# Kernel optimization log

Hardware: AMD Instinct MI355X
Metric: run time of the kernel (lower is better)

Reference implementation:

```python
import jax, jax.numpy as jnp
import numpy as np

LAT = (4, 24, 24, 24, 24, 3, 3)  # [mu, L0, L1, L2, L3, 3, 3]


def setup_inputs() -> dict:
    key = jax.random.key(0)
    k1, k2 = jax.random.split(key)
    U_re = jax.random.normal(k1, LAT, dtype=jnp.float32)
    U_im = jax.random.normal(k2, LAT, dtype=jnp.float32)
    return {"U_re": U_re, "U_im": U_im}


def _polyakov_dir(Umu, axis, L):
    """P(x) = prod_{k=0}^{L-1} U_mu(x + k*mu_hat) via a sequential scan of
    batched 3x3 complex matmuls. Umu: [L0,L1,L2,L3,3,3] complex."""

    def step(carry, _):
        P, Ush = carry
        Ush = jnp.roll(Ush, -1, axis=axis)  # U_mu(x + (k)*mu_hat)
        P = jnp.einsum('...ij,...jk->...ik', P, Ush)
        return (P, Ush), None

    (P, _), _ = jax.lax.scan(step, (Umu, Umu), None, length=L - 1)
    return P


def reference(U_re, U_im):
    U = jax.lax.complex(U_re, U_im)  # complex64 link field
    loops = jnp.stack([
        _polyakov_dir(U[mu], mu, U.shape[1 + mu]) for mu in range(4)
    ])  # [4, L0, L1, L2, L3, 3, 3] complex
    # return real/imag stacked so output is a real array
    return jnp.stack([loops.real, loops.imag])
```

## Files before the change

kernel.cpp:

```cpp
#include <hip/hip_runtime.h>

#define LSIZE 24
#define VOL (LSIZE*LSIZE*LSIZE*LSIZE)
#define NLINES (LSIZE*LSIZE*LSIZE)
#define CHUNK 3
#define TPL 8
#define LPB 32
#define TPB 256

__device__ __forceinline__ void cmul(const float* __restrict__ ar, const float* __restrict__ ai,
                                     const float* __restrict__ br, const float* __restrict__ bi,
                                     float* __restrict__ or_, float* __restrict__ oi_) {
#pragma unroll
  for (int i = 0; i < 3; ++i) {
#pragma unroll
    for (int j = 0; j < 3; ++j) {
      float sr = 0.f, si = 0.f;
#pragma unroll
      for (int m = 0; m < 3; ++m) {
        float x = ar[i*3+m], y = ai[i*3+m];
        float u = br[m*3+j], v = bi[m*3+j];
        sr = fmaf(x, u, sr);
        sr = fmaf(-y, v, sr);
        si = fmaf(x, v, si);
        si = fmaf(y, u, si);
      }
      or_[i*3+j] = sr;
      oi_[i*3+j] = si;
    }
  }
}

__device__ __forceinline__ void cp9(float* dr, float* di, const float* sr, const float* si) {
#pragma unroll
  for (int e = 0; e < 9; ++e) { dr[e] = sr[e]; di[e] = si[e]; }
}

__device__ __forceinline__ void setid(float* r, float* im) {
#pragma unroll
  for (int e = 0; e < 9; ++e) { r[e] = (e == 0 || e == 4 || e == 8) ? 1.f : 0.f; im[e] = 0.f; }
}

__device__ __forceinline__ void shup(float* dr, float* di, const float* sr, const float* si, int delta) {
#pragma unroll
  for (int e = 0; e < 9; ++e) {
    dr[e] = __shfl_up(sr[e], (unsigned)delta, 64);
    di[e] = __shfl_up(si[e], (unsigned)delta, 64);
  }
}
__device__ __forceinline__ void shdn(float* dr, float* di, const float* sr, const float* si, int delta) {
#pragma unroll
  for (int e = 0; e < 9; ++e) {
    dr[e] = __shfl_down(sr[e], (unsigned)delta, 64);
    di[e] = __shfl_down(si[e], (unsigned)delta, 64);
  }
}

__global__ __launch_bounds__(TPB, 2) void polyakov_chunk(
    const float* __restrict__ U_re, const float* __restrict__ U_im,
    float* __restrict__ out) {
  const int lane = threadIdx.x & 63;
  const int wv   = threadIdx.x >> 6;
  const int lineBase = blockIdx.x * LPB + wv * (64 / TPL);
  const int mu = lineBase / NLINES;

  int tl, ll, sh;
  if (mu == 3) { tl = lane & 7; ll = lane >> 3; sh = 1; }
  else         { tl = lane >> 3; ll = lane & 7; sh = 8; }

  const int L  = lineBase + ll;
  const int l  = L - mu * NLINES;
  const int cC = l % LSIZE;
  const int cB = (l / LSIZE) % LSIZE;
  const int cA = l / (LSIZE*LSIZE);

  int x0, x1, x2, x3, st;
  if (mu == 0)      { x0 = 0;  x1 = cA; x2 = cB; x3 = cC; st = LSIZE*LSIZE*LSIZE; }
  else if (mu == 1) { x0 = cA; x1 = 0;  x2 = cB; x3 = cC; st = LSIZE*LSIZE; }
  else if (mu == 2) { x0 = cA; x1 = cB; x2 = 0;  x3 = cC; st = LSIZE; }
  else              { x0 = cA; x1 = cB; x2 = cC; x3 = 0;  st = 1; }
  const int s0 = ((x0*LSIZE + x1)*LSIZE + x2)*LSIZE + x3;
  const int k0 = tl * CHUNK;

  const float* __restrict__ bR = U_re + (size_t)mu * (VOL*9);
  const float* __restrict__ bI = U_im + (size_t)mu * (VOL*9);

  float U0r[9], U0i[9], U1r[9], U1i[9], U2r[9], U2i[9];
  {
    const float* p = bR + (size_t)(s0 + (k0+0)*st) * 9;
    const float* q = bI + (size_t)(s0 + (k0+0)*st) * 9;
#pragma unroll
    for (int e = 0; e < 9; ++e) { U0r[e] = p[e]; U0i[e] = q[e]; }
  }
  {
    const float* p = bR + (size_t)(s0 + (k0+1)*st) * 9;
    const float* q = bI + (size_t)(s0 + (k0+1)*st) * 9;
#pragma unroll
    for (int e = 0; e < 9; ++e) { U1r[e] = p[e]; U1i[e] = q[e]; }
  }
  {
    const float* p = bR + (size_t)(s0 + (k0+2)*st) * 9;
    const float* q = bI + (size_t)(s0 + (k0+2)*st) * 9;
#pragma unroll
    for (int e = 0; e < 9; ++e) { U2r[e] = p[e]; U2i[e] = q[e]; }
  }

  float A1r[9], A1i[9], Br[9], Bi[9], S1r[9], S1i[9];
  cmul(U0r, U0i, U1r, U1i, A1r, A1i);
  cmul(A1r, A1i, U2r, U2i, Br,  Bi);
  cmul(U1r, U1i, U2r, U2i, S1r, S1i);

  float Tr[9], Ti[9], Yr[9], Yi[9];

  float Xr[9], Xi[9];
  cp9(Xr, Xi, Br, Bi);
#pragma unroll
  for (int d = 1; d < TPL; d <<= 1) {
    shup(Yr, Yi, Xr, Xi, d * sh);
    if (tl >= d) { cmul(Yr, Yi, Xr, Xi, Tr, Ti); cp9(Xr, Xi, Tr, Ti); }
  }

  float Zr[9], Zi[9];
  cp9(Zr, Zi, Br, Bi);
#pragma unroll
  for (int d = 1; d < TPL; d <<= 1) {
    shdn(Yr, Yi, Zr, Zi, d * sh);
    if (tl + d < TPL) { cmul(Zr, Zi, Yr, Yi, Tr, Ti); cp9(Zr, Zi, Tr, Ti); }
  }

  float Pr[9], Pi[9], Qr[9], Qi[9];
  shup(Pr, Pi, Xr, Xi, sh);
  if (tl == 0) setid(Pr, Pi);
  shdn(Qr, Qi, Zr, Zi, sh);
  if (tl == TPL - 1) setid(Qr, Qi);

  float Rr[9], Ri[9];
  cmul(Qr, Qi, Pr, Pi, Rr, Ri);

  float* oR = out + (size_t)mu * (VOL*9);
  float* oI = out + (size_t)(4 + mu) * (VOL*9);
  float Wr[9], Wi[9];

  cmul(Br, Bi, Rr, Ri, Tr, Ti);
  {
    float* pr = oR + (size_t)(s0 + (k0+0)*st) * 9;
    float* pi = oI + (size_t)(s0 + (k0+0)*st) * 9;
#pragma unroll
    for (int e = 0; e < 9; ++e) { pr[e] = Tr[e]; pi[e] = Ti[e]; }
  }
  cmul(Rr, Ri, U0r, U0i, Tr, Ti);
  cmul(S1r, S1i, Tr, Ti, Wr, Wi);
  {
    float* pr = oR + (size_t)(s0 + (k0+1)*st) * 9;
    float* pi = oI + (size_t)(s0 + (k0+1)*st) * 9;
#pragma unroll
    for (int e = 0; e < 9; ++e) { pr[e] = Wr[e]; pi[e] = Wi[e]; }
  }
  cmul(Rr, Ri, A1r, A1i, Tr, Ti);
  cmul(U2r, U2i, Tr, Ti, Wr, Wi);
  {
    float* pr = oR + (size_t)(s0 + (k0+2)*st) * 9;
    float* pi = oI + (size_t)(s0 + (k0+2)*st) * 9;
#pragma unroll
    for (int e = 0; e < 9; ++e) { pr[e] = Wr[e]; pi[e] = Wi[e]; }
  }
}

extern "C" void kernel_launch(void* const* d_in, const int* in_sizes, int n_in,
                              void* d_out, int out_size, void* d_ws, size_t ws_size,
                              hipStream_t stream) {
  const float* U_re = (const float*)d_in[0];
  const float* U_im = (const float*)d_in[1];
  float* out = (float*)d_out;
  int nblocks = 4 * NLINES / LPB;
  hipLaunchKernelGGL(polyakov_chunk, dim3(nblocks), dim3(TPB), 0, stream, U_re, U_im, out);
}
```

Measured before the change: 197.0 us.

## Stage outputs through LDS for coalesced stores and reload links to cut registers

For mu 0-2, each wave writes its 3x3 results into padded shared memory and then stores them so that adjacent lanes write contiguous 9-float runs, instead of each thread writing strided 36-byte chunks. The link matrices are reloaded from global memory after the scan rather than held in registers across it, and launch bounds rise to 4 blocks per CU to raise occupancy. The cost is extra LDS traffic, waitcnt barriers and repeated global loads, which the cache should mostly serve.

```diff
diff --git a/kernel.cpp b/kernel.cpp
--- a/kernel.cpp
+++ b/kernel.cpp
@@ -3,10 +3,10 @@
 #define LSIZE 24
 #define VOL (LSIZE*LSIZE*LSIZE*LSIZE)
 #define NLINES (LSIZE*LSIZE*LSIZE)
-#define CHUNK 3
-#define TPL 8
 #define LPB 32
 #define TPB 256
+#define ESTRIDE 71
+#define BUFW (18*ESTRIDE)
 
 __device__ __forceinline__ void cmul(const float* __restrict__ ar, const float* __restrict__ ai,
                                      const float* __restrict__ br, const float* __restrict__ bi,
@@ -56,20 +56,21 @@
   }
 }
 
-__global__ __launch_bounds__(TPB, 2) void polyakov_chunk(
+__global__ __launch_bounds__(TPB, 4) void polyakov_hyb(
     const float* __restrict__ U_re, const float* __restrict__ U_im,
     float* __restrict__ out) {
+  __shared__ float buf[4 * BUFW];
+
   const int lane = threadIdx.x & 63;
   const int wv   = threadIdx.x >> 6;
-  const int lineBase = blockIdx.x * LPB + wv * (64 / TPL);
-  const int mu = lineBase / NLINES;
+  const int mu   = (blockIdx.x * LPB) / NLINES;
 
   int tl, ll, sh;
   if (mu == 3) { tl = lane & 7; ll = lane >> 3; sh = 1; }
   else         { tl = lane >> 3; ll = lane & 7; sh = 8; }
 
-  const int L  = lineBase + ll;
-  const int l  = L - mu * NLINES;
+  const int l0 = blockIdx.x * LPB + wv * 8 - mu * NLINES;
+  const int l  = l0 + ll;
   const int cC = l % LSIZE;
   const int cB = (l / LSIZE) % LSIZE;
   const int cA = l / (LSIZE*LSIZE);
@@ -80,90 +81,112 @@
   else if (mu == 2) { x0 = cA; x1 = cB; x2 = 0;  x3 = cC; st = LSIZE; }
   else              { x0 = cA; x1 = cB; x2 = cC; x3 = 0;  st = 1; }
   const int s0 = ((x0*LSIZE + x1)*LSIZE + x2)*LSIZE + x3;
-  const int k0 = tl * CHUNK;
-
-  const float* __restrict__ bR = U_re + (size_t)mu * (VOL*9);
-  const float* __restrict__ bI = U_im + (size_t)mu * (VOL*9);
-
-  float U0r[9], U0i[9], U1r[9], U1i[9], U2r[9], U2i[9];
+  const int k0 = 3 * tl;
+
+  const float* __restrict__ gR = U_re + (size_t)mu * (VOL*9);
+  const float* __restrict__ gI = U_im + (size_t)mu * (VOL*9);
+  float* __restrict__ oR = out + (size_t)mu * (VOL*9);
+  float* __restrict__ oI = out + (size_t)(4 + mu) * (VOL*9);
+
+  auto ldU = [&](int kk, float* r, float* im_) {
+    const float* p = gR + (size_t)(s0 + kk*st) * 9;
+    const float* q = gI + (size_t)(s0 + kk*st) * 9;
+#pragma unroll
+    for (int e = 0; e < 9; ++e) { r[e] = p[e]; im_[e] = q[e]; }
+  };
+
+  float* wbuf = buf + wv * BUFW;
+
+  auto emit = [&](const float* Vr, const float* Vi, int j) {
+    if (mu == 3) {
+      float* pr = oR + (size_t)(s0 + (k0 + j) * st) * 9;
+      float* pi = oI + (size_t)(s0 + (k0 + j) * st) * 9;
+#pragma unroll
+      for (int e = 0; e < 9; ++e) { pr[e] = Vr[e]; pi[e] = Vi[e]; }
+    } else {
+      asm volatile("s_waitcnt lgkmcnt(0)" ::: "memory");
+#pragma unroll
+      for (int e = 0; e < 9; ++e) {
+        wbuf[e * ESTRIDE + lane]       = Vr[e];
+        wbuf[(9 + e) * ESTRIDE + lane] = Vi[e];
+      }
+      asm volatile("s_waitcnt lgkmcnt(0)" ::: "memory");
+      __builtin_amdgcn_sched_barrier(0);
+      const int s0w = s0 - ll;
+      int slab = 0, rem = lane;
+#pragma unroll
+      for (int p = 0; p < 9; ++p) {
+        int line8 = rem / 9;
+        int e = rem - line8 * 9;
+        int m = (slab << 3) + line8;
+        float vr = wbuf[e * ESTRIDE + m];
+        float vi = wbuf[(9 + e) * ESTRIDE + m];
+        size_t off = (size_t)(s0w + (3 * slab + j) * st) * 9 + rem;
+        oR[off] = vr;
+        oI[off] = vi;
+        int rem2 = rem + 64;
+        int c = rem2 >= 72;
+        rem = c ? rem2 - 72 : rem2;
+        slab += c;
+      }
+    }
+  };
+
+  float Br[9], Bi[9];
   {
-    const float* p = bR + (size_t)(s0 + (k0+0)*st) * 9;
-    const float* q = bI + (size_t)(s0 + (k0+0)*st) * 9;
-#pragma unroll
-    for (int e = 0; e < 9; ++e) { U0r[e] = p[e]; U0i[e] = q[e]; }
-  }
+    float Ar[9], Ai[9], Cr[9], Ci[9], Tr0[9], Ti0[9];
+    ldU(k0 + 0, Ar, Ai);
+    ldU(k0 + 1, Cr, Ci);
+    cmul(Ar, Ai, Cr, Ci, Tr0, Ti0);
+    ldU(k0 + 2, Ar, Ai);
+    cmul(Tr0, Ti0, Ar, Ai, Br, Bi);
+  }
+
+  float Yr[9], Yi[9], Tr[9], Ti[9];
+
+  float Pr[9], Pi[9];
   {
-    const float* p = bR + (size_t)(s0 + (k0+1)*st) * 9;
-    const float* q = bI + (size_t)(s0 + (k0+1)*st) * 9;
-#pragma unroll
-    for (int e = 0; e < 9; ++e) { U1r[e] = p[e]; U1i[e] = q[e]; }
-  }
+    float Xr[9], Xi[9];
+    cp9(Xr, Xi, Br, Bi);
+#pragma unroll
+    for (int d = 1; d < 8; d <<= 1) {
+      shup(Yr, Yi, Xr, Xi, d * sh);
+      if (tl >= d) { cmul(Yr, Yi, Xr, Xi, Tr, Ti); cp9(Xr, Xi, Tr, Ti); }
+    }
+    shup(Pr, Pi, Xr, Xi, sh);
+    if (tl == 0) setid(Pr, Pi);
+  }
+
+  float Rr[9], Ri[9];
   {
-    const float* p = bR + (size_t)(s0 + (k0+2)*st) * 9;
-    const float* q = bI + (size_t)(s0 + (k0+2)*st) * 9;
-#pragma unroll
-    for (int e = 0; e < 9; ++e) { U2r[e] = p[e]; U2i[e] = q[e]; }
-  }
-
-  float A1r[9], A1i[9], Br[9], Bi[9], S1r[9], S1i[9];
-  cmul(U0r, U0i, U1r, U1i, A1r, A1i);
-  cmul(A1r, A1i, U2r, U2i, Br,  Bi);
-  cmul(U1r, U1i, U2r, U2i, S1r, S1i);
-
-  float Tr[9], Ti[9], Yr[9], Yi[9];
-
-  float Xr[9], Xi[9];
-  cp9(Xr, Xi, Br, Bi);
-#pragma unroll
-  for (int d = 1; d < TPL; d <<= 1) {
-    shup(Yr, Yi, Xr, Xi, d * sh);
-    if (tl >= d) { cmul(Yr, Yi, Xr, Xi, Tr, Ti); cp9(Xr, Xi, Tr, Ti); }
-  }
-
-  float Zr[9], Zi[9];
-  cp9(Zr, Zi, Br, Bi);
-#pragma unroll
-  for (int d = 1; d < TPL; d <<= 1) {
-    shdn(Yr, Yi, Zr, Zi, d * sh);
-    if (tl + d < TPL) { cmul(Zr, Zi, Yr, Yi, Tr, Ti); cp9(Zr, Zi, Tr, Ti); }
-  }
-
-  float Pr[9], Pi[9], Qr[9], Qi[9];
-  shup(Pr, Pi, Xr, Xi, sh);
-  if (tl == 0) setid(Pr, Pi);
-  shdn(Qr, Qi, Zr, Zi, sh);
-  if (tl == TPL - 1) setid(Qr, Qi);
-
-  float Rr[9], Ri[9];
-  cmul(Qr, Qi, Pr, Pi, Rr, Ri);
-
-  float* oR = out + (size_t)mu * (VOL*9);
-  float* oI = out + (size_t)(4 + mu) * (VOL*9);
-  float Wr[9], Wi[9];
+    float Zr[9], Zi[9];
+    cp9(Zr, Zi, Br, Bi);
+#pragma unroll
+    for (int d = 1; d < 8; d <<= 1) {
+      shdn(Yr, Yi, Zr, Zi, d * sh);
+      if (tl + d < 8) { cmul(Zr, Zi, Yr, Yi, Tr, Ti); cp9(Zr, Zi, Tr, Ti); }
+    }
+    shdn(Yr, Yi, Zr, Zi, sh);
+    if (tl == 7) setid(Yr, Yi);
+    cmul(Yr, Yi, Pr, Pi, Rr, Ri);
+  }
 
   cmul(Br, Bi, Rr, Ri, Tr, Ti);
-  {
-    float* pr = oR + (size_t)(s0 + (k0+0)*st) * 9;
-    float* pi = oI + (size_t)(s0 + (k0+0)*st) * 9;
-#pragma unroll
-    for (int e = 0; e < 9; ++e) { pr[e] = Tr[e]; pi[e] = Ti[e]; }
-  }
-  cmul(Rr, Ri, U0r, U0i, Tr, Ti);
-  cmul(S1r, S1i, Tr, Ti, Wr, Wi);
-  {
-    float* pr = oR + (size_t)(s0 + (k0+1)*st) * 9;
-    float* pi = oI + (size_t)(s0 + (k0+1)*st) * 9;
-#pragma unroll
-    for (int e = 0; e < 9; ++e) { pr[e] = Wr[e]; pi[e] = Wi[e]; }
-  }
-  cmul(Rr, Ri, A1r, A1i, Tr, Ti);
-  cmul(U2r, U2i, Tr, Ti, Wr, Wi);
-  {
-    float* pr = oR + (size_t)(s0 + (k0+2)*st) * 9;
-    float* pi = oI + (size_t)(s0 + (k0+2)*st) * 9;
-#pragma unroll
-    for (int e = 0; e < 9; ++e) { pr[e] = Wr[e]; pi[e] = Wi[e]; }
-  }
+  emit(Tr, Ti, 0);
+
+  float W2r[9], W2i[9], U1r[9], U1i[9];
+  ldU(k0 + 2, Yr, Yi);
+  cmul(Yr, Yi, Rr, Ri, W2r, W2i);
+  ldU(k0 + 1, U1r, U1i);
+  float W1r[9], W1i[9];
+  cmul(U1r, U1i, W2r, W2i, W1r, W1i);
+  ldU(k0 + 0, Pr, Pi);
+
+  cmul(W1r, W1i, Pr, Pi, Tr, Ti);
+  emit(Tr, Ti, 1);
+  cmul(W2r, W2i, Pr, Pi, Yr, Yi);
+  cmul(Yr, Yi, U1r, U1i, Tr, Ti);
+  emit(Tr, Ti, 2);
 }
 
 extern "C" void kernel_launch(void* const* d_in, const int* in_sizes, int n_in,
@@ -173,5 +196,5 @@
   const float* U_im = (const float*)d_in[1];
   float* out = (float*)d_out;
   int nblocks = 4 * NLINES / LPB;
-  hipLaunchKernelGGL(polyakov_chunk, dim3(nblocks), dim3(TPB), 0, stream, U_re, U_im, out);
-}
+  hipLaunchKernelGGL(polyakov_hyb, dim3(nblocks), dim3(TPB), 0, stream, U_re, U_im, out);
+}
```

After: 212.6 us. 1.08x slower.
